# Kernel tuning notes

Hardware: AMD Instinct MI355X
Metric: run time of the kernel (lower is better)

The kernel has to match this reference:

```python
import jax, jax.numpy as jnp
import numpy as np

B, C, H, W = 32, 256, 32, 32   # batch, channels (inplanes==planes), spatial
E = 8                          # num_experts
EPS = 1e-5                     # BatchNorm eps


def setup_inputs() -> dict:
    key = jax.random.key(0)
    ks = jax.random.split(key, 6)
    s = 0.05
    return {
        "x": jax.random.normal(ks[0], (B, C, H, W), dtype=jnp.float32),
        # router: GAP -> Linear(C, E) -> sigmoid
        "router_w": jax.random.normal(ks[1], (E, C), dtype=jnp.float32) * s,
        "router_b": jnp.zeros((E,), dtype=jnp.float32),
        # expert kernel banks for the two CondConv2d layers (OIHW per expert)
        "w1": jax.random.normal(ks[2], (E, C, C, 3, 3), dtype=jnp.float32) * s,
        "w2": jax.random.normal(ks[3], (E, C, C, 3, 3), dtype=jnp.float32) * s,
        # BatchNorm (eval mode: running stats) params for bn1/bn2
        "g1": jnp.ones((C,), jnp.float32), "b1": jnp.zeros((C,), jnp.float32),
        "m1": jnp.zeros((C,), jnp.float32), "v1": jnp.ones((C,), jnp.float32),
        "g2": jnp.ones((C,), jnp.float32), "b2": jnp.zeros((C,), jnp.float32),
        "m2": jnp.zeros((C,), jnp.float32), "v2": jnp.ones((C,), jnp.float32),
    }


def _bn(x, g, b, m, v):
    # eval-mode BatchNorm over channel dim 1
    scale = (g * jax.lax.rsqrt(v + EPS))[None, :, None, None]
    shift = (b - m * g * jax.lax.rsqrt(v + EPS))[None, :, None, None]
    return x * scale + shift


def _cond_conv(x, w_bank, r):
    # x: [B,C,H,W]; w_bank: [E,O,I,3,3]; r: [B,E]
    # combine expert kernels per sample, then per-sample 3x3 conv (pad=1, stride=1)
    k = jnp.einsum('be,eoihw->boihw', r, w_bank)  # [B,O,I,3,3]

    def one(xb, kb):
        return jax.lax.conv_general_dilated(
            xb[None], kb, window_strides=(1, 1), padding=[(1, 1), (1, 1)],
            dimension_numbers=('NCHW', 'OIHW', 'NCHW'))[0]

    return jax.vmap(one)(x, k)  # [B,O,H,W]


def reference(x, router_w, router_b, w1, w2, g1, b1, m1, v1, g2, b2, m2, v2):
    # BasicRouter: global average pool -> linear -> sigmoid
    r = jax.nn.sigmoid(jnp.mean(x, axis=(2, 3)) @ router_w.T + router_b)  # [B,E]
    # drop_expert is identity in eval mode (training=False)
    out = jax.nn.relu(_bn(_cond_conv(x, w1, r), g1, b1, m1, v1))
    out = _bn(_cond_conv(out, w2, r), g2, b2, m2, v2)
    return jax.nn.relu(out + x)  # identity residual (stride=1, inplanes==planes)
```

## Files before the change

### kernel.cpp

```cpp
#include <hip/hip_runtime.h>

typedef unsigned short ushort_t;
typedef __attribute__((ext_vector_type(8))) __bf16 bf16x8;
typedef __attribute__((ext_vector_type(4))) float f32x4;
typedef __attribute__((ext_vector_type(4))) int i32x4;
typedef __attribute__((ext_vector_type(4))) unsigned short u16x4;

#define BN_EPS 1e-5f
#define EPAD 136

__device__ __forceinline__ ushort_t f2bf(float f) {
    union { float f; unsigned u; } v; v.f = f;
    unsigned r = v.u + 0x7FFFu + ((v.u >> 16) & 1u);
    return (ushort_t)(r >> 16);
}
__device__ __forceinline__ float bf2f(ushort_t h) {
    union { unsigned u; float f; } v; v.u = ((unsigned)h) << 16; return v.f;
}

__device__ __forceinline__ void async_cp16(const ushort_t* g, ushort_t* l) {
    __builtin_amdgcn_global_load_lds(
        (const __attribute__((address_space(1))) unsigned int*)g,
        (__attribute__((address_space(3))) unsigned int*)l, 16, 0, 0);
}

__global__ void transpose_gap_kernel(const float* __restrict__ x, ushort_t* __restrict__ xt,
                                     float* __restrict__ gapsum) {
    __shared__ float tile[32][33];
    int b = blockIdx.z, c0 = blockIdx.y * 32, p0 = blockIdx.x * 32;
    int tx = threadIdx.x & 31, ty = threadIdx.x >> 5;
    float ps[4];
    #pragma unroll
    for (int i = 0; i < 4; ++i) {
        int c = ty + i * 8;
        float v = x[((long)b * 256 + c0 + c) * 1024 + p0 + tx];
        tile[c][tx] = v;
        ps[i] = v;
    }
    #pragma unroll
    for (int off = 16; off; off >>= 1)
        #pragma unroll
        for (int i = 0; i < 4; ++i) ps[i] += __shfl_down(ps[i], off, 32);
    if (tx == 0)
        #pragma unroll
        for (int i = 0; i < 4; ++i) atomicAdd(&gapsum[b * 256 + c0 + ty + i * 8], ps[i]);
    __syncthreads();
    #pragma unroll
    for (int i = 0; i < 4; ++i) {
        int p = ty + i * 8;
        xt[((long)b * 1024 + p0 + p) * 256 + c0 + tx] = f2bf(tile[tx][p]);
    }
}

__global__ void router_linear_kernel(const float* __restrict__ gapsum, const float* __restrict__ rw,
                                     const float* __restrict__ rb, float* __restrict__ r) {
    int t = threadIdx.x, b = t >> 3, e = t & 7;
    float s = 0.f;
    for (int c = 0; c < 256; ++c) s += gapsum[b * 256 + c] * rw[e * 256 + c];
    r[t] = 1.f / (1.f + expf(-(s * (1.f / 1024.f) + rb[e])));
}

__global__ void combine_kernel(const float* __restrict__ w, const float* __restrict__ r,
                               ushort_t* __restrict__ ko) {
    int g = blockIdx.x * 256 + threadIdx.x;
    int b0 = blockIdx.y * 8;
    float wv[8][9];
    #pragma unroll
    for (int e = 0; e < 8; ++e)
        #pragma unroll
        for (int p = 0; p < 9; ++p)
            wv[e][p] = w[((long)e * 65536 + g) * 9 + p];
    for (int bb = 0; bb < 8; ++bb) {
        int b = b0 + bb;
        float rv[8];
        #pragma unroll
        for (int e = 0; e < 8; ++e) rv[e] = r[b * 8 + e];
        #pragma unroll
        for (int p = 0; p < 9; ++p) {
            float s = 0.f;
            #pragma unroll
            for (int e = 0; e < 8; ++e) s += rv[e] * wv[e][p];
            ko[((long)(b * 9 + p)) * 65536 + g] = f2bf(s);
        }
    }
}

template <int MODE>
__global__ __launch_bounds__(256, 2) void gemm_conv(
    const ushort_t* __restrict__ xin,
    const ushort_t* __restrict__ kbank,
    void* __restrict__ outp,
    const float* __restrict__ gam, const float* __restrict__ bet,
    const float* __restrict__ mu, const float* __restrict__ var,
    const ushort_t* __restrict__ residt) {
    __shared__ ushort_t smem[29440];
    ushort_t* ldsB = smem;
    ushort_t* ldsA = smem + 13056;

    const int t = threadIdx.x;
    const int lane = t & 63;
    const int lane15 = lane & 15;
    const int quad = lane >> 4;
    const int wv = t >> 6;
    const int id = blockIdx.x;
    const int q  = id >> 3;
    const int mt = q & 1;
    const int nt = (q >> 1) & 7;
    const int b  = (id & 7) + ((q >> 4) << 3);
    const int h0 = nt * 4;
    const int p0 = nt * 128;
    const int mw0 = (wv >> 1) * 64;
    const int nw0 = (wv & 1) * 64;
    const int wbase = t & ~63;

    f32x4 acc[4][4];
    #pragma unroll
    for (int i = 0; i < 4; ++i)
        #pragma unroll
        for (int j = 0; j < 4; ++j) acc[i][j] = 0.f;

    if (t < 96) {
        int rix = t >> 3, j = t & 7;
        int pi = (rix >> 1) * 34 + (rix & 1) * 33;
        i32x4 z = 0;
        *(i32x4*)(&ldsB[(pi * 8 + j) * 8]) = z;
    }
    if (nt == 0) { i32x4 z = 0; *(i32x4*)(&ldsB[(8 + t) * 8]) = z; }
    if (nt == 7) { i32x4 z = 0; *(i32x4*)(&ldsB[((5 * 34 + 1) * 8 + t) * 8]) = z; }

    const long xbase = (long)b * 1024 * 256;
    const long kbase = (long)b * 9 * 65536;

    auto stageB = [&](int kc) {
        #pragma unroll
        for (int hh = 0; hh < 6; ++hh) {
            int hg = h0 + hh - 1;
            if (hg < 0 || hg >= 32) continue;
            int ww = t >> 3;
            int pi = hh * 34 + 1 + ww;
            int jd = (t & 7) ^ (pi & 7);
            async_cp16(xin + xbase + (long)(hg * 32 + ww) * 256 + kc * 64 + jd * 8,
                       ldsB + ((hh * 34 + 1) * 8 + wbase) * 8);
        }
    };
    auto stageA = [&](int kc, int pos, int buf) {
        const ushort_t* srcA = kbank + kbase + (long)pos * 65536 + (long)mt * 32768 + kc * 64;
        ushort_t* base = ldsA + buf * 8192;
        #pragma unroll
        for (int it = 0; it < 4; ++it) {
            int s = it * 256 + t;
            int row = s >> 3;
            int k8 = (s & 7) ^ (row & 7);
            async_cp16(srcA + (long)row * 256 + k8 * 8, base + (it * 256 + wbase) * 8);
        }
    };

    stageB(0);
    stageA(0, 0, 0);
    __syncthreads();

    int par = 0;
    for (int kc = 0; kc < 4; ++kc) {
        for (int pos = 0; pos < 9; ++pos) {
            if (!(kc == 3 && pos == 8)) {
                int nk = kc, np = pos + 1;
                if (np == 9) { np = 0; ++nk; }
                stageA(nk, np, par ^ 1);
            }
            const int dh = pos / 3 - 1, dw = pos % 3 - 1;
            const ushort_t* ab = ldsA + par * 8192;
            #pragma unroll
            for (int kb = 0; kb < 2; ++kb) {
                int jk = kb * 4 + quad;
                bf16x8 af[4], bfr[4];
                #pragma unroll
                for (int mf = 0; mf < 4; ++mf) {
                    int row = mw0 + mf * 16 + lane15;
                    af[mf] = *(const bf16x8*)(ab + (row * 8 + (jk ^ (row & 7))) * 8);
                }
                #pragma unroll
                for (int nf = 0; nf < 4; ++nf) {
                    int n = nw0 + nf * 16 + lane15;
                    int pi = ((n >> 5) + 1 + dh) * 34 + (n & 31) + 1 + dw;
                    bfr[nf] = *(const bf16x8*)(&ldsB[(pi * 8 + (jk ^ (pi & 7))) * 8]);
                }
                #pragma unroll
                for (int mf = 0; mf < 4; ++mf)
                    #pragma unroll
                    for (int nf = 0; nf < 4; ++nf)
                        acc[mf][nf] = __builtin_amdgcn_mfma_f32_16x16x32_bf16(af[mf], bfr[nf], acc[mf][nf], 0, 0, 0);
            }
            __syncthreads();
            if (pos == 8 && kc < 3) { stageB(kc + 1); __syncthreads(); }
            par ^= 1;
        }
    }

    u16x4 rres[4][4];
    if (MODE == 1) {
        #pragma unroll
        for (int mf = 0; mf < 4; ++mf)
            #pragma unroll
            for (int nf = 0; nf < 4; ++nf) {
                int p = p0 + nw0 + nf * 16 + lane15;
                int cb = mt * 128 + mw0 + mf * 16 + quad * 4;
                rres[mf][nf] = *(const u16x4*)(residt + ((long)b * 1024 + p) * 256 + cb);
            }
    }

    float sc[4][4], sh[4][4];
    #pragma unroll
    for (int mf = 0; mf < 4; ++mf)
        #pragma unroll
        for (int i = 0; i < 4; ++i) {
            int c = mt * 128 + mw0 + mf * 16 + quad * 4 + i;
            float s = gam[c] * rsqrtf(var[c] + BN_EPS);
            sc[mf][i] = s;
            sh[mf][i] = bet[c] - mu[c] * s;
        }

    if (MODE == 0) {
        __syncthreads();
        ushort_t* ldsE = smem;
        #pragma unroll
        for (int mf = 0; mf < 4; ++mf)
            #pragma unroll
            for (int nf = 0; nf < 4; ++nf) {
                int pl = nw0 + nf * 16 + lane15;
                int cb = mw0 + mf * 16 + quad * 4;
                u16x4 pk;
                #pragma unroll
                for (int i = 0; i < 4; ++i) {
                    float v = acc[mf][nf][i] * sc[mf][i] + sh[mf][i];
                    pk[i] = f2bf(fmaxf(v, 0.f));
                }
                *(u16x4*)(&ldsE[pl * EPAD + cb]) = pk;
            }
        __syncthreads();
        ushort_t* op = (ushort_t*)outp;
        #pragma unroll
        for (int it = 0; it < 8; ++it) {
            int s = t + it * 256;
            int row = s >> 4, l16 = s & 15;
            i32x4 v = *(i32x4*)(&ldsE[row * EPAD + l16 * 8]);
            *(i32x4*)(op + ((long)b * 1024 + p0 + row) * 256 + mt * 128 + l16 * 8) = v;
        }
    } else {
        float* op = (float*)outp;
        #pragma unroll
        for (int mf = 0; mf < 4; ++mf)
            #pragma unroll
            for (int nf = 0; nf < 4; ++nf) {
                int p = p0 + nw0 + nf * 16 + lane15;
                #pragma unroll
                for (int i = 0; i < 4; ++i) {
                    int c = mt * 128 + mw0 + mf * 16 + quad * 4 + i;
                    float v = acc[mf][nf][i] * sc[mf][i] + sh[mf][i] + bf2f(rres[mf][nf][i]);
                    op[((long)b * 256 + c) * 1024 + p] = fmaxf(v, 0.f);
                }
            }
    }
}

extern "C" void kernel_launch(void* const* d_in, const int* in_sizes, int n_in,
                              void* d_out, int out_size, void* d_ws, size_t ws_size,
                              hipStream_t stream) {
    const float* x  = (const float*)d_in[0];
    const float* rw = (const float*)d_in[1];
    const float* rb = (const float*)d_in[2];
    const float* w1 = (const float*)d_in[3];
    const float* w2 = (const float*)d_in[4];
    const float* g1 = (const float*)d_in[5];
    const float* b1 = (const float*)d_in[6];
    const float* m1 = (const float*)d_in[7];
    const float* v1 = (const float*)d_in[8];
    const float* g2 = (const float*)d_in[9];
    const float* b2 = (const float*)d_in[10];
    const float* m2 = (const float*)d_in[11];
    const float* v2 = (const float*)d_in[12];

    const size_t GAP_OFF = 4096;
    const size_t XT_OFF  = 36864;
    const size_t O1_OFF  = XT_OFF + (size_t)16777216;
    const size_t KB_OFF  = O1_OFF + (size_t)16777216;
    const size_t NEED    = KB_OFF + (size_t)32 * 9 * 65536 * 2;
    if (ws_size < NEED) return;

    char* ws = (char*)d_ws;
    float* r       = (float*)ws;
    float* gapsum  = (float*)(ws + GAP_OFF);
    ushort_t* xt   = (ushort_t*)(ws + XT_OFF);
    ushort_t* o1   = (ushort_t*)(ws + O1_OFF);
    ushort_t* kbuf = (ushort_t*)(ws + KB_OFF);

    hipMemsetAsync(gapsum, 0, 32768, stream);
    transpose_gap_kernel<<<dim3(32, 8, 32), 256, 0, stream>>>(x, xt, gapsum);
    router_linear_kernel<<<1, 256, 0, stream>>>(gapsum, rw, rb, r);
    combine_kernel<<<dim3(256, 4), 256, 0, stream>>>(w1, r, kbuf);
    gemm_conv<0><<<512, 256, 0, stream>>>(xt, kbuf, (void*)o1, g1, b1, m1, v1, nullptr);
    combine_kernel<<<dim3(256, 4), 256, 0, stream>>>(w2, r, kbuf);
    gemm_conv<1><<<512, 256, 0, stream>>>(o1, kbuf, d_out, g2, b2, m2, v2, xt);
}
```

Measured before the change: 254.3 us.

## Fuse router into combine and fold second-layer kernel combine into first conv

Removes the separate single-block router kernel by having each combine block compute its own sigmoid router weights in shared memory. The second layer's per-sample expert weight combine is appended to the tail of the first conv kernel, writing into a second workspace buffer when enough workspace exists. This saves two launches and a serial dependency, and LDS fragment offsets in the conv inner loop are precomputed once and XOR-ed per k-half. In exchange the router dot product is recomputed redundantly in every block, the conv kernel gets a longer, register-heavy tail that may cost occupancy, and an extra 37 MB of workspace is needed.

```diff
diff --git a/kernel.cpp b/kernel.cpp
--- a/kernel.cpp
+++ b/kernel.cpp
@@ -52,29 +52,33 @@
     }
 }
 
-__global__ void router_linear_kernel(const float* __restrict__ gapsum, const float* __restrict__ rw,
-                                     const float* __restrict__ rb, float* __restrict__ r) {
-    int t = threadIdx.x, b = t >> 3, e = t & 7;
-    float s = 0.f;
-    for (int c = 0; c < 256; ++c) s += gapsum[b * 256 + c] * rw[e * 256 + c];
-    r[t] = 1.f / (1.f + expf(-(s * (1.f / 1024.f) + rb[e])));
-}
-
-__global__ void combine_kernel(const float* __restrict__ w, const float* __restrict__ r,
-                               ushort_t* __restrict__ ko) {
-    int g = blockIdx.x * 256 + threadIdx.x;
-    int b0 = blockIdx.y * 8;
+__global__ void combine_router_kernel(const float* __restrict__ w, const float* __restrict__ gapsum,
+                                      const float* __restrict__ rw, const float* __restrict__ rb,
+                                      ushort_t* __restrict__ ko) {
+    __shared__ float rsh[16][8];
+    int t = threadIdx.x;
+    int g = blockIdx.x * 256 + t;
+    int b0 = blockIdx.y * 16;
+    if (t < 128) {
+        int bb = t >> 3, e = t & 7;
+        const float* gp = &gapsum[(b0 + bb) * 256];
+        const float* wp = &rw[e * 256];
+        float s = 0.f;
+        for (int c = 0; c < 256; ++c) s += gp[c] * wp[c];
+        rsh[bb][e] = 1.f / (1.f + expf(-(s * (1.f / 1024.f) + rb[e])));
+    }
     float wv[8][9];
     #pragma unroll
     for (int e = 0; e < 8; ++e)
         #pragma unroll
         for (int p = 0; p < 9; ++p)
             wv[e][p] = w[((long)e * 65536 + g) * 9 + p];
-    for (int bb = 0; bb < 8; ++bb) {
+    __syncthreads();
+    for (int bb = 0; bb < 16; ++bb) {
         int b = b0 + bb;
         float rv[8];
         #pragma unroll
-        for (int e = 0; e < 8; ++e) rv[e] = r[b * 8 + e];
+        for (int e = 0; e < 8; ++e) rv[e] = rsh[bb][e];
         #pragma unroll
         for (int p = 0; p < 9; ++p) {
             float s = 0.f;
@@ -85,14 +89,17 @@
     }
 }
 
-template <int MODE>
+template <int MODE, int FUSE>
 __global__ __launch_bounds__(256, 2) void gemm_conv(
     const ushort_t* __restrict__ xin,
     const ushort_t* __restrict__ kbank,
     void* __restrict__ outp,
     const float* __restrict__ gam, const float* __restrict__ bet,
     const float* __restrict__ mu, const float* __restrict__ var,
-    const ushort_t* __restrict__ residt) {
+    const ushort_t* __restrict__ residt,
+    const float* __restrict__ w2raw, const float* __restrict__ gapsum,
+    const float* __restrict__ rw, const float* __restrict__ rb,
+    ushort_t* __restrict__ k2out) {
     __shared__ ushort_t smem[29440];
     ushort_t* ldsB = smem;
     ushort_t* ldsA = smem + 13056;
@@ -155,6 +162,13 @@
         }
     };
 
+    int aoff[4];
+    #pragma unroll
+    for (int mf = 0; mf < 4; ++mf) {
+        int row = mw0 + mf * 16 + lane15;
+        aoff[mf] = (row * 8 + (quad ^ (row & 7))) * 8;
+    }
+
     stageB(0);
     stageA(0, 0, 0);
     __syncthreads();
@@ -169,21 +183,23 @@
             }
             const int dh = pos / 3 - 1, dw = pos % 3 - 1;
             const ushort_t* ab = ldsA + par * 8192;
+            int boff[4];
+            #pragma unroll
+            for (int nf = 0; nf < 4; ++nf) {
+                int n = nw0 + nf * 16 + lane15;
+                int pi = ((n >> 5) + 1 + dh) * 34 + (n & 31) + 1 + dw;
+                boff[nf] = (pi * 8 + (quad ^ (pi & 7))) * 8;
+            }
             #pragma unroll
             for (int kb = 0; kb < 2; ++kb) {
-                int jk = kb * 4 + quad;
+                const int kx = kb ? 32 : 0;
                 bf16x8 af[4], bfr[4];
                 #pragma unroll
-                for (int mf = 0; mf < 4; ++mf) {
-                    int row = mw0 + mf * 16 + lane15;
-                    af[mf] = *(const bf16x8*)(ab + (row * 8 + (jk ^ (row & 7))) * 8);
-                }
-                #pragma unroll
-                for (int nf = 0; nf < 4; ++nf) {
-                    int n = nw0 + nf * 16 + lane15;
-                    int pi = ((n >> 5) + 1 + dh) * 34 + (n & 31) + 1 + dw;
-                    bfr[nf] = *(const bf16x8*)(&ldsB[(pi * 8 + (jk ^ (pi & 7))) * 8]);
-                }
+                for (int mf = 0; mf < 4; ++mf)
+                    af[mf] = *(const bf16x8*)(ab + (aoff[mf] ^ kx));
+                #pragma unroll
+                for (int nf = 0; nf < 4; ++nf)
+                    bfr[nf] = *(const bf16x8*)(ldsB + (boff[nf] ^ kx));
                 #pragma unroll
                 for (int mf = 0; mf < 4; ++mf)
                     #pragma unroll
@@ -259,6 +275,41 @@
                     op[((long)b * 256 + c) * 1024 + p] = fmaxf(v, 0.f);
                 }
             }
+    }
+
+    if (FUSE) {
+        __syncthreads();
+        float* rsh = (float*)smem;
+        {
+            int bb = t >> 3, e = t & 7;
+            const float* gp = &gapsum[bb * 256];
+            const float* wp = &rw[e * 256];
+            float s = 0.f;
+            for (int c = 0; c < 256; ++c) s += gp[c] * wp[c];
+            rsh[bb * 8 + e] = 1.f / (1.f + expf(-(s * (1.f / 1024.f) + rb[e])));
+        }
+        __syncthreads();
+        int gg = id * 128 + (t & 127);
+        int b0 = (t >> 7) * 16;
+        float wv2[8][9];
+        #pragma unroll
+        for (int e = 0; e < 8; ++e)
+            #pragma unroll
+            for (int p = 0; p < 9; ++p)
+                wv2[e][p] = w2raw[((long)e * 65536 + gg) * 9 + p];
+        for (int bb = 0; bb < 16; ++bb) {
+            int bq = b0 + bb;
+            float rv[8];
+            #pragma unroll
+            for (int e = 0; e < 8; ++e) rv[e] = rsh[bq * 8 + e];
+            #pragma unroll
+            for (int p = 0; p < 9; ++p) {
+                float s = 0.f;
+                #pragma unroll
+                for (int e = 0; e < 8; ++e) s += rv[e] * wv2[e][p];
+                k2out[((long)(bq * 9 + p)) * 65536 + gg] = f2bf(s);
+            }
+        }
     }
 }
 
@@ -279,25 +330,34 @@
     const float* m2 = (const float*)d_in[11];
     const float* v2 = (const float*)d_in[12];
 
-    const size_t GAP_OFF = 4096;
-    const size_t XT_OFF  = 36864;
+    const size_t XT_OFF  = 32768;
     const size_t O1_OFF  = XT_OFF + (size_t)16777216;
     const size_t KB_OFF  = O1_OFF + (size_t)16777216;
-    const size_t NEED    = KB_OFF + (size_t)32 * 9 * 65536 * 2;
-    if (ws_size < NEED) return;
+    const size_t KSZ     = (size_t)32 * 9 * 65536 * 2;
+    const size_t NEED1   = KB_OFF + KSZ;
+    const size_t NEED2   = NEED1 + KSZ;
+    if (ws_size < NEED1) return;
 
     char* ws = (char*)d_ws;
-    float* r       = (float*)ws;
-    float* gapsum  = (float*)(ws + GAP_OFF);
-    ushort_t* xt   = (ushort_t*)(ws + XT_OFF);
-    ushort_t* o1   = (ushort_t*)(ws + O1_OFF);
-    ushort_t* kbuf = (ushort_t*)(ws + KB_OFF);
+    float* gapsum   = (float*)ws;
+    ushort_t* xt    = (ushort_t*)(ws + XT_OFF);
+    ushort_t* o1    = (ushort_t*)(ws + O1_OFF);
+    ushort_t* kbuf  = (ushort_t*)(ws + KB_OFF);
+    ushort_t* kbuf2 = (ushort_t*)(ws + NEED1);
 
     hipMemsetAsync(gapsum, 0, 32768, stream);
     transpose_gap_kernel<<<dim3(32, 8, 32), 256, 0, stream>>>(x, xt, gapsum);
-    router_linear_kernel<<<1, 256, 0, stream>>>(gapsum, rw, rb, r);
-    combine_kernel<<<dim3(256, 4), 256, 0, stream>>>(w1, r, kbuf);
-    gemm_conv<0><<<512, 256, 0, stream>>>(xt, kbuf, (void*)o1, g1, b1, m1, v1, nullptr);
-    combine_kernel<<<dim3(256, 4), 256, 0, stream>>>(w2, r, kbuf);
-    gemm_conv<1><<<512, 256, 0, stream>>>(o1, kbuf, d_out, g2, b2, m2, v2, xt);
-}
+    combine_router_kernel<<<dim3(256, 2), 256, 0, stream>>>(w1, gapsum, rw, rb, kbuf);
+    if (ws_size >= NEED2) {
+        gemm_conv<0, 1><<<512, 256, 0, stream>>>(xt, kbuf, (void*)o1, g1, b1, m1, v1, nullptr,
+                                                 w2, gapsum, rw, rb, kbuf2);
+        gemm_conv<1, 0><<<512, 256, 0, stream>>>(o1, kbuf2, d_out, g2, b2, m2, v2, xt,
+                                                 nullptr, nullptr, nullptr, nullptr, nullptr);
+    } else {
+        gemm_conv<0, 0><<<512, 256, 0, stream>>>(xt, kbuf, (void*)o1, g1, b1, m1, v1, nullptr,
+                                                 nullptr, nullptr, nullptr, nullptr, nullptr);
+        combine_router_kernel<<<dim3(256, 2), 256, 0, stream>>>(w2, gapsum, rw, rb, kbuf);
+        gemm_conv<1, 0><<<512, 256, 0, stream>>>(o1, kbuf, d_out, g2, b2, m2, v2, xt,
+                                                 nullptr, nullptr, nullptr, nullptr, nullptr);
+    }
+}
```

After: 293.3 us. 15.3% more time.

## Fuse router linear into expert-combine kernel and combine both layers in one launch

Applied to the files above, without the earlier changes.

The router linear+sigmoid is recomputed per block into shared memory inside the combine kernel, which removes a separate single-block launch. Each weight element is now loaded once and reused across all 32 batch samples instead of being reloaded for every group of 8. When workspace permits, both layers' combined kernel banks are produced by a single launch into separate buffers. The cost is that every block redundantly computes the 256x8 router dot products, and the path needs twice the kernel-bank workspace.

```diff
diff --git a/kernel.cpp b/kernel.cpp
--- a/kernel.cpp
+++ b/kernel.cpp
@@ -52,35 +52,44 @@
     }
 }
 
-__global__ void router_linear_kernel(const float* __restrict__ gapsum, const float* __restrict__ rw,
-                                     const float* __restrict__ rb, float* __restrict__ r) {
-    int t = threadIdx.x, b = t >> 3, e = t & 7;
-    float s = 0.f;
-    for (int c = 0; c < 256; ++c) s += gapsum[b * 256 + c] * rw[e * 256 + c];
-    r[t] = 1.f / (1.f + expf(-(s * (1.f / 1024.f) + rb[e])));
-}
-
-__global__ void combine_kernel(const float* __restrict__ w, const float* __restrict__ r,
-                               ushort_t* __restrict__ ko) {
-    int g = blockIdx.x * 256 + threadIdx.x;
-    int b0 = blockIdx.y * 8;
-    float wv[8][9];
+__global__ __launch_bounds__(256, 4) void combine_kernel2(
+    const float* __restrict__ w1, const float* __restrict__ w2,
+    const float* __restrict__ gapsum,
+    const float* __restrict__ rw, const float* __restrict__ rb,
+    ushort_t* __restrict__ k1, ushort_t* __restrict__ k2) {
+    const float* w = blockIdx.z ? w2 : w1;
+    ushort_t* ko = blockIdx.z ? k2 : k1;
+    __shared__ float rsh[32][8];
+    int t = threadIdx.x;
+    {
+        int bb = t >> 3, e = t & 7;
+        const float* gp = &gapsum[bb * 256];
+        const float* wp = &rw[e * 256];
+        float s = 0.f;
+        for (int c = 0; c < 256; ++c) s += gp[c] * wp[c];
+        rsh[bb][e] = 1.f / (1.f + expf(-(s * (1.f / 1024.f) + rb[e])));
+    }
+    int gl = t & 127, ph = t >> 7;
+    long g = (long)blockIdx.x * 128 + gl;
+    int pbase = ph ? 4 : 0, np = ph ? 5 : 4;
+    float wv[5][8];
     #pragma unroll
     for (int e = 0; e < 8; ++e)
-        #pragma unroll
-        for (int p = 0; p < 9; ++p)
-            wv[e][p] = w[((long)e * 65536 + g) * 9 + p];
-    for (int bb = 0; bb < 8; ++bb) {
-        int b = b0 + bb;
+        for (int p = 0; p < np; ++p)
+            wv[p][e] = w[((long)e * 65536 + g) * 9 + pbase + p];
+    __syncthreads();
+    for (int b = 0; b < 32; ++b) {
         float rv[8];
         #pragma unroll
-        for (int e = 0; e < 8; ++e) rv[e] = r[b * 8 + e];
-        #pragma unroll
-        for (int p = 0; p < 9; ++p) {
-            float s = 0.f;
-            #pragma unroll
-            for (int e = 0; e < 8; ++e) s += rv[e] * wv[e][p];
-            ko[((long)(b * 9 + p)) * 65536 + g] = f2bf(s);
+        for (int e = 0; e < 8; ++e) rv[e] = rsh[b][e];
+        #pragma unroll
+        for (int p = 0; p < 5; ++p) {
+            if (p < np) {
+                float s = 0.f;
+                #pragma unroll
+                for (int e = 0; e < 8; ++e) s += rv[e] * wv[p][e];
+                ko[((long)(b * 9 + pbase + p)) * 65536 + g] = f2bf(s);
+            }
         }
     }
 }
@@ -279,25 +288,31 @@
     const float* m2 = (const float*)d_in[11];
     const float* v2 = (const float*)d_in[12];
 
-    const size_t GAP_OFF = 4096;
-    const size_t XT_OFF  = 36864;
+    const size_t XT_OFF  = 32768;
     const size_t O1_OFF  = XT_OFF + (size_t)16777216;
     const size_t KB_OFF  = O1_OFF + (size_t)16777216;
-    const size_t NEED    = KB_OFF + (size_t)32 * 9 * 65536 * 2;
-    if (ws_size < NEED) return;
+    const size_t KSZ     = (size_t)32 * 9 * 65536 * 2;
+    const size_t NEED1   = KB_OFF + KSZ;
+    const size_t NEED2   = NEED1 + KSZ;
+    if (ws_size < NEED1) return;
 
     char* ws = (char*)d_ws;
-    float* r       = (float*)ws;
-    float* gapsum  = (float*)(ws + GAP_OFF);
-    ushort_t* xt   = (ushort_t*)(ws + XT_OFF);
-    ushort_t* o1   = (ushort_t*)(ws + O1_OFF);
-    ushort_t* kbuf = (ushort_t*)(ws + KB_OFF);
+    float* gapsum   = (float*)ws;
+    ushort_t* xt    = (ushort_t*)(ws + XT_OFF);
+    ushort_t* o1    = (ushort_t*)(ws + O1_OFF);
+    ushort_t* kbuf  = (ushort_t*)(ws + KB_OFF);
+    ushort_t* kbuf2 = (ushort_t*)(ws + NEED1);
 
     hipMemsetAsync(gapsum, 0, 32768, stream);
     transpose_gap_kernel<<<dim3(32, 8, 32), 256, 0, stream>>>(x, xt, gapsum);
-    router_linear_kernel<<<1, 256, 0, stream>>>(gapsum, rw, rb, r);
-    combine_kernel<<<dim3(256, 4), 256, 0, stream>>>(w1, r, kbuf);
-    gemm_conv<0><<<512, 256, 0, stream>>>(xt, kbuf, (void*)o1, g1, b1, m1, v1, nullptr);
-    combine_kernel<<<dim3(256, 4), 256, 0, stream>>>(w2, r, kbuf);
-    gemm_conv<1><<<512, 256, 0, stream>>>(o1, kbuf, d_out, g2, b2, m2, v2, xt);
-}
+    if (ws_size >= NEED2) {
+        combine_kernel2<<<dim3(512, 1, 2), 256, 0, stream>>>(w1, w2, gapsum, rw, rb, kbuf, kbuf2);
+        gemm_conv<0><<<512, 256, 0, stream>>>(xt, kbuf, (void*)o1, g1, b1, m1, v1, nullptr);
+        gemm_conv<1><<<512, 256, 0, stream>>>(o1, kbuf2, d_out, g2, b2, m2, v2, xt);
+    } else {
+        combine_kernel2<<<dim3(512, 1, 1), 256, 0, stream>>>(w1, w1, gapsum, rw, rb, kbuf, kbuf);
+        gemm_conv<0><<<512, 256, 0, stream>>>(xt, kbuf, (void*)o1, g1, b1, m1, v1, nullptr);
+        combine_kernel2<<<dim3(512, 1, 1), 256, 0, stream>>>(w2, w2, gapsum, rw, rb, kbuf, kbuf);
+        gemm_conv<1><<<512, 256, 0, stream>>>(o1, kbuf, d_out, g2, b2, m2, v2, xt);
+    }
+}
```

Measured after the change: 302.2 us. 1.19x slower.
